# Kernel optimization log

Measured on AMD Instinct MI355X. Metric: run time of the kernel, lower is better.

## Reference

```python
import jax, jax.numpy as jnp
import numpy as np

B, S, HID = 8, 4096, 1024
NH, HD = 16, 64  # heads, head_dim
LN_EPS = 1e-12


def setup_inputs() -> dict:
    key = jax.random.key(0)
    ks = jax.random.split(key, 12)
    sd = 1.0 / np.sqrt(HID)
    return {
        "input_tensor": jax.random.normal(ks[0], (B, S, HID), jnp.float32),
        "attention_mask": jnp.ones((B, S), jnp.int32),
        "ln_gamma": jnp.ones((HID,), jnp.float32),
        "ln_beta": jnp.zeros((HID,), jnp.float32),
        "Wq": jax.random.normal(ks[1], (HID, HID), jnp.float32) * sd,
        "bq": jnp.zeros((HID,), jnp.float32),
        "Wk": jax.random.normal(ks[2], (HID, HID), jnp.float32) * sd,
        "bk": jnp.zeros((HID,), jnp.float32),
        "Wv": jax.random.normal(ks[3], (HID, HID), jnp.float32) * sd,
        "bv": jnp.zeros((HID,), jnp.float32),
        "Wo": jax.random.normal(ks[4], (HID, HID), jnp.float32) * sd,
        "bo": jnp.zeros((HID,), jnp.float32),
    }


def _layernorm(x, g, b):
    mu = jnp.mean(x, axis=-1, keepdims=True)
    var = jnp.mean(jnp.square(x - mu), axis=-1, keepdims=True)
    return (x - mu) * jax.lax.rsqrt(var + LN_EPS) * g + b


def reference(input_tensor, attention_mask, ln_gamma, ln_beta,
              Wq, bq, Wk, bk, Wv, bv, Wo, bo):
    # NOTE: attention_mask is accepted but unused, matching the original module.
    x = input_tensor
    x_norm = _layernorm(x, ln_gamma, ln_beta)
    # projections: query from normalized input, key/value from raw input
    q = (x_norm @ Wq.T + bq).reshape(B, S, NH, HD).transpose(0, 2, 1, 3)  # bhsd
    k = (x @ Wk.T + bk).reshape(B, S, NH, HD).transpose(0, 2, 1, 3)      # bhsd
    v = (x @ Wv.T + bv).reshape(B, S, NH, HD).transpose(0, 2, 1, 3)      # bhsd

    eq = jax.nn.elu(q)
    ek = jax.nn.elu(k)
    # per-token L2 norms over head_dim (matches norm over d in both layouts)
    eq = eq / jnp.linalg.norm(eq, axis=-1, keepdims=True)
    ek = ek / jnp.linalg.norm(ek, axis=-1, keepdims=True)

    # linear attention: Q (K^T V), never materializing [S,S]
    kv = jnp.einsum('bhsd,bhse->bhde', ek, v)          # [B,H,d,d]
    ctx = jnp.einsum('bhsd,bhde->bhse', eq, kv) / np.sqrt(HD)

    ctx = ctx.transpose(0, 2, 1, 3).reshape(B, S, HID)
    out = ctx @ Wo.T + bo
    return out + x  # residual (dropouts are identity in eval mode)
```

## Files before the change

kernel.cpp:

```cpp
#include <hip/hip_runtime.h>

typedef unsigned short u16;
typedef unsigned int   u32;
typedef __attribute__((ext_vector_type(8))) __bf16 bf16x8;
typedef __attribute__((ext_vector_type(4))) float  f32x4;

#define BQ   8
#define SQ   4096
#define NHQ  16
#define HIDD 1024
#define TOKN 32768

__device__ __forceinline__ u16 f2bf(float f){
  u32 u = __builtin_bit_cast(u32, f);
  u += 0x7fffu + ((u >> 16) & 1u);
  return (u16)(u >> 16);
}
__device__ __forceinline__ float bf2f(u16 h){
  return __builtin_bit_cast(float, (u32)h << 16);
}
__device__ __forceinline__ void gl16(const void* g, void* l){
  __builtin_amdgcn_global_load_lds((const __attribute__((address_space(1))) void*)g,
                                   (__attribute__((address_space(3))) void*)l, 16, 0, 0);
}
#define MFMA(a,b,c) __builtin_amdgcn_mfma_f32_16x16x32_bf16((a),(b),(c),0,0,0)

__global__ __launch_bounds__(256) void k_cast4(const float* __restrict__ wq,
    const float* __restrict__ wk, const float* __restrict__ wv, const float* __restrict__ wo,
    u16* __restrict__ oq, u16* __restrict__ okv, u16* __restrict__ oo){
  const int sel = blockIdx.x >> 10;
  const int i = ((blockIdx.x & 1023) << 8) + threadIdx.x;
  const float* in = (sel == 0) ? wq : (sel == 1) ? wk : (sel == 2) ? wv : wo;
  u16* o = (sel == 0) ? oq : (sel == 1) ? okv : (sel == 2) ? (okv + 1024 * 1024) : oo;
  float4 v = ((const float4*)in)[i];
  ushort4 r;
  r.x = f2bf(v.x); r.y = f2bf(v.y); r.z = f2bf(v.z); r.w = f2bf(v.w);
  ((ushort4*)o)[i] = r;
}

__global__ __launch_bounds__(256) void k_ln(const float* __restrict__ x, const float* __restrict__ g,
    const float* __restrict__ be, u16* __restrict__ xbf, u16* __restrict__ xnbf){
  const int row = blockIdx.x, t = threadIdx.x;
  const float4 v = ((const float4*)(x + (size_t)row * HIDD))[t];
  float s  = v.x + v.y + v.z + v.w;
  float ss = v.x*v.x + v.y*v.y + v.z*v.z + v.w*v.w;
  #pragma unroll
  for (int o = 1; o < 64; o <<= 1){ s += __shfl_xor(s, o); ss += __shfl_xor(ss, o); }
  __shared__ float sm[8];
  const int lane = t & 63, wid = t >> 6;
  if (lane == 0){ sm[wid] = s; sm[wid + 4] = ss; }
  __syncthreads();
  s  = sm[0] + sm[1] + sm[2] + sm[3];
  ss = sm[4] + sm[5] + sm[6] + sm[7];
  const float mu   = s * (1.f / 1024.f);
  const float var  = ss * (1.f / 1024.f) - mu * mu;
  const float rstd = rsqrtf(var + 1e-12f);
  const float4 gg = ((const float4*)g)[t];
  const float4 bb = ((const float4*)be)[t];
  ushort4 xo, no;
  xo.x = f2bf(v.x); no.x = f2bf((v.x - mu) * rstd * gg.x + bb.x);
  xo.y = f2bf(v.y); no.y = f2bf((v.y - mu) * rstd * gg.y + bb.y);
  xo.z = f2bf(v.z); no.z = f2bf((v.z - mu) * rstd * gg.z + bb.z);
  xo.w = f2bf(v.w); no.w = f2bf((v.w - mu) * rstd * gg.w + bb.w);
  ((ushort4*)(xbf  + (size_t)row * HIDD))[t] = xo;
  ((ushort4*)(xnbf + (size_t)row * HIDD))[t] = no;
}

struct GP {
  const u16* A; const u16* W; const float* b1; const float* b2;
  int nsplit, lgNB, LDC, nblk; u16* outb;
};

template<int RES>
__global__ __launch_bounds__(512, 2) void k_gemm256(GP p0, GP p1, int seg0,
    const float* __restrict__ resid, float* __restrict__ outf){
  __shared__ union {
    u16 st[2][2][16384];
    float cep[8][1056];
  } sm;

  const GP& p = (blockIdx.x < seg0) ? p0 : p1;
  const int bseg = (blockIdx.x < seg0) ? blockIdx.x : blockIdx.x - seg0;
  const u16* __restrict__ A = p.A;
  const u16* __restrict__ W = p.W;
  const int lgNB = p.lgNB, LDC = p.LDC;

  const int wg = ((bseg & 7) * (p.nblk >> 3)) + (bseg >> 3);
  const int m0 = (wg >> lgNB) << 8;
  const int n0 = (wg & ((1 << lgNB) - 1)) << 8;

  const int t = threadIdx.x, lane = t & 63, wid = t >> 6;
  const int ln15 = lane & 15, hi = lane >> 4;
  const int wr = wid >> 2, wc = wid & 3;
  const int lg = lane & 7, lr = lane >> 3;

  auto stage = [&](int buf, int op, const u16* __restrict__ src, int rowoff, int kt){
    #pragma unroll
    for (int i = 0; i < 4; i++){
      const int cb  = ((i << 3) + wid) << 6;
      const int row = (cb >> 3) + lr;
      const int g   = lg ^ lr;
      gl16(src + (size_t)(rowoff + row) * HIDD + (kt << 6) + (g << 3),
           &sm.st[buf][op][cb << 3]);
    }
  };
  #define RD_A(c,m,ks) (*(const bf16x8*)&sm.st[c][0][(((wr << 7) + ((m) << 4) + ln15) << 6) + \
      (((((ks) << 2) + hi) ^ (lane & 7)) << 3)])
  #define RD_B(c,n,ks) (*(const bf16x8*)&sm.st[c][1][(((wc << 6) + ((n) << 4) + ln15) << 6) + \
      (((((ks) << 2) + hi) ^ (lane & 7)) << 3)])

  f32x4 acc[8][4] = {};

  stage(0, 0, A, m0, 0);
  stage(0, 1, W, n0, 0);
  stage(1, 1, W, n0, 1);
  asm volatile("s_waitcnt vmcnt(4)" ::: "memory");
  __builtin_amdgcn_s_barrier();
  asm volatile("" ::: "memory");

  const int NT = HIDD / 64;
  for (int kt = 0; kt < NT; ++kt){
    const int c = kt & 1;
    bf16x8 af[4][2], bq[4][2];
    #pragma unroll
    for (int m = 0; m < 4; m++){ af[m][0] = RD_A(c, m, 0); af[m][1] = RD_A(c, m, 1); }
    #pragma unroll
    for (int n = 0; n < 4; n++){ bq[n][0] = RD_B(c, n, 0); bq[n][1] = RD_B(c, n, 1); }
    const int ka = kt + 1 < NT ? kt + 1 : NT - 1;
    stage(c ^ 1, 0, A, m0, ka);
    __builtin_amdgcn_s_setprio(1);
    #pragma unroll
    for (int m = 0; m < 4; m++)
      #pragma unroll
      for (int n = 0; n < 4; n++){
        acc[m][n] = MFMA(af[m][0], bq[n][0], acc[m][n]);
        acc[m][n] = MFMA(af[m][1], bq[n][1], acc[m][n]);
      }
    __builtin_amdgcn_s_setprio(0);
    asm volatile("" ::: "memory");
    __builtin_amdgcn_s_barrier();
    asm volatile("" ::: "memory");
    #pragma unroll
    for (int m = 0; m < 4; m++){ af[m][0] = RD_A(c, m + 4, 0); af[m][1] = RD_A(c, m + 4, 1); }
    const int kb = kt + 2 < NT ? kt + 2 : NT - 1;
    stage(c, 1, W, n0, kb);
    __builtin_amdgcn_s_setprio(1);
    #pragma unroll
    for (int m = 0; m < 4; m++)
      #pragma unroll
      for (int n = 0; n < 4; n++){
        acc[m + 4][n] = MFMA(af[m][0], bq[n][0], acc[m + 4][n]);
        acc[m + 4][n] = MFMA(af[m][1], bq[n][1], acc[m + 4][n]);
      }
    __builtin_amdgcn_s_setprio(0);
    asm volatile("s_waitcnt vmcnt(4)" ::: "memory");
    __builtin_amdgcn_s_barrier();
    asm volatile("" ::: "memory");
  }
  #undef RD_A
  #undef RD_B

  asm volatile("s_waitcnt vmcnt(0)" ::: "memory");
  __builtin_amdgcn_s_barrier();
  asm volatile("" ::: "memory");

  const float* bp = (n0 < p.nsplit) ? p.b1 : (p.b2 - p.nsplit);
  float bn[4];
  #pragma unroll
  for (int n = 0; n < 4; n++) bn[n] = bp[n0 + (wc << 6) + (n << 4) + ln15];

  if constexpr (RES){
    #pragma unroll
    for (int m = 0; m < 8; m++)
      #pragma unroll
      for (int n = 0; n < 4; n++)
        #pragma unroll
        for (int r = 0; r < 4; r++){
          int row = m0 + (wr << 7) + (m << 4) + (hi << 2) + r;
          int col = n0 + (wc << 6) + (n << 4) + ln15;
          outf[(size_t)row * LDC + col] = acc[m][n][r] + bn[n]
                                        + resid[(size_t)row * HIDD + col];
        }
  } else {
    float* cw = &sm.cep[wid][0];
    const int rr = lane >> 3, cb8 = (lane & 7) << 3;
    u16* outb = p.outb;
    #pragma unroll
    for (int m = 0; m < 8; m++){
      #pragma unroll
      for (int n = 0; n < 4; n++)
        #pragma unroll
        for (int r = 0; r < 4; r++)
          cw[((hi << 2) + r) * 66 + (n << 4) + ln15] = acc[m][n][r] + bn[n];
      #pragma unroll
      for (int j = 0; j < 2; j++){
        const int row = (j << 3) + rr;
        u32 ro[4];
        #pragma unroll
        for (int pq = 0; pq < 4; pq++){
          float v0 = cw[row * 66 + cb8 + 2 * pq];
          float v1 = cw[row * 66 + cb8 + 2 * pq + 1];
          ro[pq] = (u32)f2bf(v0) | ((u32)f2bf(v1) << 16);
        }
        uint4 o; o.x = ro[0]; o.y = ro[1]; o.z = ro[2]; o.w = ro[3];
        *(uint4*)&outb[(size_t)(m0 + (wr << 7) + (m << 4) + row) * LDC
                       + n0 + (wc << 6) + cb8] = o;
      }
    }
  }
}

__global__ __launch_bounds__(256) void k_elunorm(u16* __restrict__ q){
  size_t idx = (size_t)blockIdx.x * 256 + threadIdx.x;
  uint4 u = ((const uint4*)q)[idx];
  u32 uu[4] = {u.x, u.y, u.z, u.w};
  float e[8]; float ss = 0.f;
  #pragma unroll
  for (int i = 0; i < 4; i++){
    float f0 = bf2f((u16)(uu[i] & 0xffff));
    float f1 = bf2f((u16)(uu[i] >> 16));
    f0 = f0 > 0.f ? f0 : expm1f(f0);
    f1 = f1 > 0.f ? f1 : expm1f(f1);
    e[2*i] = f0; e[2*i+1] = f1;
    ss += f0 * f0 + f1 * f1;
  }
  ss += __shfl_xor(ss, 1); ss += __shfl_xor(ss, 2); ss += __shfl_xor(ss, 4);
  float rn = rsqrtf(ss);
  u32 ro[4];
  #pragma unroll
  for (int i = 0; i < 4; i++)
    ro[i] = (u32)f2bf(e[2*i] * rn) | ((u32)f2bf(e[2*i+1] * rn) << 16);
  uint4 o; o.x = ro[0]; o.y = ro[1]; o.z = ro[2]; o.w = ro[3];
  ((uint4*)q)[idx] = o;
}

__global__ __launch_bounds__(256) void k_transpose2(const u16* __restrict__ kvb,
                                                    u16* __restrict__ ekT, u16* __restrict__ vT){
  __shared__ float tile[64][65];
  __shared__ float pr[64][4];
  __shared__ float rn[64];
  const int sb = blockIdx.x << 6, h2 = blockIdx.y, b = blockIdx.z;
  const int h = h2 & 15;
  const int isK = (h2 >> 4) == 0;
  const u16* in = kvb + ((h2 >> 4) << 10);
  u16* outp = isK ? ekT : vT;
  const int t = threadIdx.x;
  {
    const int tok = t >> 2, q = t & 3;
    const u16* src = in + (size_t)(b * SQ + sb + tok) * 2048 + (h << 6) + (q << 4);
    uint4 u0 = *(const uint4*)src;
    uint4 u1 = *(const uint4*)(src + 8);
    u32 uu[8] = {u0.x, u0.y, u0.z, u0.w, u1.x, u1.y, u1.z, u1.w};
    float ss = 0.f;
    #pragma unroll
    for (int i = 0; i < 8; i++){
      float f0 = bf2f((u16)(uu[i] & 0xffff));
      float f1 = bf2f((u16)(uu[i] >> 16));
      if (isK){
        f0 = f0 > 0.f ? f0 : expm1f(f0);
        f1 = f1 > 0.f ? f1 : expm1f(f1);
        ss += f0 * f0 + f1 * f1;
      }
      tile[tok][(q << 4) + 2*i]     = f0;
      tile[tok][(q << 4) + 2*i + 1] = f1;
    }
    if (isK) pr[tok][q] = ss;
  }
  __syncthreads();
  if (isK){
    if (t < 64) rn[t] = rsqrtf(pr[t][0] + pr[t][1] + pr[t][2] + pr[t][3]);
    __syncthreads();
  }
  const int d = t >> 2, sq2 = (t & 3) << 4;
  u16* dst = outp + ((size_t)(b * NHQ + h) * 64 + d) * SQ + sb + sq2;
  u32 ro[8];
  #pragma unroll
  for (int i = 0; i < 8; i++){
    float v0 = tile[sq2 + 2*i][d];
    float v1 = tile[sq2 + 2*i + 1][d];
    if (isK){ v0 *= rn[sq2 + 2*i]; v1 *= rn[sq2 + 2*i + 1]; }
    ro[i] = (u32)f2bf(v0) | ((u32)f2bf(v1) << 16);
  }
  uint4 o0; o0.x = ro[0]; o0.y = ro[1]; o0.z = ro[2]; o0.w = ro[3];
  uint4 o1; o1.x = ro[4]; o1.y = ro[5]; o1.z = ro[6]; o1.w = ro[7];
  *(uint4*)dst = o0;
  *(uint4*)(dst + 8) = o1;
}

__global__ __launch_bounds__(256) void k_kv(const u16* __restrict__ vT, const u16* __restrict__ ekT,
                                            u16* __restrict__ kvT){
  const int bh = blockIdx.x;
  const u16* Av = vT  + (size_t)bh * 64 * SQ;
  const u16* Bk = ekT + (size_t)bh * 64 * SQ;
  const int lane = threadIdx.x & 63, wid = threadIdx.x >> 6;
  const int ln15 = lane & 15, hi = lane >> 4;
  f32x4 acc[4][4] = {};
  const int kb = wid << 10;
  for (int ks = 0; ks < 32; ++ks){
    const int k0 = kb + (ks << 5) + (hi << 3);
    bf16x8 af[4], bfr[4];
    #pragma unroll
    for (int m = 0; m < 4; m++) af[m]  = *(const bf16x8*)(Av + (size_t)((m << 4) + ln15) * SQ + k0);
    #pragma unroll
    for (int n = 0; n < 4; n++) bfr[n] = *(const bf16x8*)(Bk + (size_t)((n << 4) + ln15) * SQ + k0);
    #pragma unroll
    for (int m = 0; m < 4; m++)
      #pragma unroll
      for (int n = 0; n < 4; n++)
        acc[m][n] = MFMA(af[m], bfr[n], acc[m][n]);
  }
  __shared__ float red[64][64];
  for (int w = 0; w < 4; ++w){
    if (wid == w){
      #pragma unroll
      for (int m = 0; m < 4; m++)
        #pragma unroll
        for (int n = 0; n < 4; n++)
          #pragma unroll
          for (int r = 0; r < 4; r++){
            int row = (m << 4) + (hi << 2) + r;
            int col = (n << 4) + ln15;
            if (w == 0) red[row][col] = acc[m][n][r];
            else        red[row][col] += acc[m][n][r];
          }
    }
    __syncthreads();
  }
  u16* dst = kvT + (size_t)bh * 4096;
  const int tt = threadIdx.x;
  #pragma unroll
  for (int i = 0; i < 16; i++){
    int idx = tt * 16 + i;
    dst[idx] = f2bf(red[idx >> 6][idx & 63] * 0.125f);
  }
}

__global__ __launch_bounds__(256) void k_ctx(const u16* __restrict__ eq, const u16* __restrict__ kvT,
                                             u16* __restrict__ ctx){
  __shared__ u16 Alds[1024 * 8];
  __shared__ u16 Blds[512 * 8];
  const int sb = blockIdx.x << 7;
  const int h = blockIdx.y, b = blockIdx.z;
  const int bh = (b << 4) + h;
  const int t = threadIdx.x, lane = t & 63, wid = t >> 6;
  const int ln15 = lane & 15, hi = lane >> 4;
  {
    uint4 va[4]; uint4 vb[2];
    #pragma unroll
    for (int i = 0; i < 4; i++){
      int c = (wid << 6) + (i << 8) + lane;
      int g = c >> 7, row = c & 127;
      va[i] = *(const uint4*)(eq + (size_t)(b * SQ + sb + row) * HIDD + (h << 6) + g * 8);
    }
    #pragma unroll
    for (int i = 0; i < 2; i++){
      int c = (wid << 6) + (i << 8) + lane;
      int g = c >> 6, row = c & 63;
      vb[i] = *(const uint4*)(kvT + (size_t)bh * 4096 + (row << 6) + g * 8);
    }
    #pragma unroll
    for (int i = 0; i < 4; i++)
      *(uint4*)&Alds[((wid << 6) + (i << 8) + lane) * 8] = va[i];
    #pragma unroll
    for (int i = 0; i < 2; i++)
      *(uint4*)&Blds[((wid << 6) + (i << 8) + lane) * 8] = vb[i];
  }
  __syncthreads();
  f32x4 acc[2][4] = {};
  #pragma unroll
  for (int k2 = 0; k2 < 2; k2++){
    const int g = (k2 << 2) + hi;
    bf16x8 af[2], bfr[4];
    #pragma unroll
    for (int m = 0; m < 2; m++) af[m]  = *(const bf16x8*)&Alds[((g << 7) + (wid << 5) + (m << 4) + ln15) * 8];
    #pragma unroll
    for (int n = 0; n < 4; n++) bfr[n] = *(const bf16x8*)&Blds[((g << 6) + (n << 4) + ln15) * 8];
    #pragma unroll
    for (int m = 0; m < 2; m++)
      #pragma unroll
      for (int n = 0; n < 4; n++)
        acc[m][n] = MFMA(af[m], bfr[n], acc[m][n]);
  }
  #pragma unroll
  for (int m = 0; m < 2; m++)
    #pragma unroll
    for (int n = 0; n < 4; n++)
      #pragma unroll
      for (int r = 0; r < 4; r++){
        int srow = sb + (wid << 5) + (m << 4) + (hi << 2) + r;
        int col  = (n << 4) + ln15;
        ctx[(size_t)(b * SQ + srow) * HIDD + (h << 6) + col] = f2bf(acc[m][n][r]);
      }
}

extern "C" void kernel_launch(void* const* d_in, const int* in_sizes, int n_in,
                              void* d_out, int out_size, void* d_ws, size_t ws_size,
                              hipStream_t stream){
  const float* x   = (const float*)d_in[0];
  const float* lng = (const float*)d_in[2];
  const float* lnb = (const float*)d_in[3];
  const float* Wq  = (const float*)d_in[4];
  const float* bq  = (const float*)d_in[5];
  const float* Wk  = (const float*)d_in[6];
  const float* bk  = (const float*)d_in[7];
  const float* Wv  = (const float*)d_in[8];
  const float* bv  = (const float*)d_in[9];
  const float* Wo  = (const float*)d_in[10];
  const float* bo  = (const float*)d_in[11];
  float* out = (float*)d_out;

  char* w = (char*)d_ws;
  const size_t MB = 1ull << 20;
  u16* wqb  = (u16*)(w + 0   * MB);
  u16* wkvb = (u16*)(w + 2   * MB);
  u16* wob  = (u16*)(w + 6   * MB);
  u16* xbf  = (u16*)(w + 8   * MB);
  u16* xnbf = (u16*)(w + 72  * MB);
  u16* qb   = (u16*)(w + 136 * MB);
  u16* kvb  = (u16*)(w + 200 * MB);
  u16* kvT  = (u16*)(w + 328 * MB);
  u16* ekT = xnbf;
  u16* vT  = xbf;
  u16* ctx = kvb;

  k_cast4<<<4096, 256, 0, stream>>>(Wq, Wk, Wv, Wo, wqb, wkvb, wob);
  k_ln<<<TOKN, 256, 0, stream>>>(x, lng, lnb, xbf, xnbf);

  GP pq  = { xnbf, wqb,  bq, bq, 1 << 30, 2, 1024, 512,  qb  };
  GP pkv = { xbf,  wkvb, bk, bv, 1024,    3, 2048, 1024, kvb };
  k_gemm256<0><<<1536, 512, 0, stream>>>(pq, pkv, 512, nullptr, nullptr);

  k_elunorm<<<16384, 256, 0, stream>>>(qb);
  k_transpose2<<<dim3(64, 32, 8), 256, 0, stream>>>(kvb, ekT, vT);
  k_kv<<<128, 256, 0, stream>>>(vT, ekT, kvT);
  k_ctx<<<dim3(32, 16, 8), 256, 0, stream>>>(qb, kvT, ctx);

  GP po = { ctx, wob, bo, bo, 1 << 30, 2, 1024, 512, nullptr };
  k_gemm256<1><<<512, 512, 0, stream>>>(po, po, 512, x, out);

  (void)in_sizes; (void)n_in; (void)out_size; (void)ws_size;
}
```

Measured before the change: 745.0 us.

## Shrink GEMM tile to 256x128 with K=32 steps for higher occupancy

Changes the bf16 MFMA GEMM from 256x256 tiles with K=64 stages to 256x128 tiles with K=32 stages. LDS drops from 64KB to 48KB, and launch bounds move to 4 blocks per CU. The grids double and the staging/swizzle, pipeline waits and epilogue are rewritten to match. The aim is more concurrent blocks and better latency hiding, at the cost of lower arithmetic intensity per tile and twice as many barriers per K.

```diff
diff --git a/kernel.cpp b/kernel.cpp
--- a/kernel.cpp
+++ b/kernel.cpp
@@ -72,11 +72,11 @@
 };
 
 template<int RES>
-__global__ __launch_bounds__(512, 2) void k_gemm256(GP p0, GP p1, int seg0,
+__global__ __launch_bounds__(512, 4) void k_gemm(GP p0, GP p1, int seg0,
     const float* __restrict__ resid, float* __restrict__ outf){
   __shared__ union {
-    u16 st[2][2][16384];
-    float cep[8][1056];
+    struct { u16 A[2][8192]; u16 B[2][4096]; } st;
+    float cep[8][544];
   } sm;
 
   const GP& p = (blockIdx.x < seg0) ? p0 : p1;
@@ -87,127 +87,104 @@
 
   const int wg = ((bseg & 7) * (p.nblk >> 3)) + (bseg >> 3);
   const int m0 = (wg >> lgNB) << 8;
-  const int n0 = (wg & ((1 << lgNB) - 1)) << 8;
+  const int n0 = (wg & ((1 << lgNB) - 1)) << 7;
 
   const int t = threadIdx.x, lane = t & 63, wid = t >> 6;
   const int ln15 = lane & 15, hi = lane >> 4;
   const int wr = wid >> 2, wc = wid & 3;
-  const int lg = lane & 7, lr = lane >> 3;
-
-  auto stage = [&](int buf, int op, const u16* __restrict__ src, int rowoff, int kt){
-    #pragma unroll
-    for (int i = 0; i < 4; i++){
-      const int cb  = ((i << 3) + wid) << 6;
-      const int row = (cb >> 3) + lr;
-      const int g   = lg ^ lr;
-      gl16(src + (size_t)(rowoff + row) * HIDD + (kt << 6) + (g << 3),
-           &sm.st[buf][op][cb << 3]);
+
+  auto stage = [&](int buf, int kt){
+    #pragma unroll
+    for (int i = 0; i < 2; i++){
+      const int c = (i << 9) + t;
+      const int row = c >> 2, g = c & 3;
+      gl16(A + (size_t)(m0 + row) * HIDD + (kt << 5) + ((g ^ (row & 3)) << 3),
+           &sm.st.A[buf][c << 3]);
+    }
+    {
+      const int c = t;
+      const int row = c >> 2, g = c & 3;
+      gl16(W + (size_t)(n0 + row) * HIDD + (kt << 5) + ((g ^ (row & 3)) << 3),
+           &sm.st.B[buf][c << 3]);
     }
   };
-  #define RD_A(c,m,ks) (*(const bf16x8*)&sm.st[c][0][(((wr << 7) + ((m) << 4) + ln15) << 6) + \
-      (((((ks) << 2) + hi) ^ (lane & 7)) << 3)])
-  #define RD_B(c,n,ks) (*(const bf16x8*)&sm.st[c][1][(((wc << 6) + ((n) << 4) + ln15) << 6) + \
-      (((((ks) << 2) + hi) ^ (lane & 7)) << 3)])
-
-  f32x4 acc[8][4] = {};
-
-  stage(0, 0, A, m0, 0);
-  stage(0, 1, W, n0, 0);
-  stage(1, 1, W, n0, 1);
-  asm volatile("s_waitcnt vmcnt(4)" ::: "memory");
-  __builtin_amdgcn_s_barrier();
-  asm volatile("" ::: "memory");
-
-  const int NT = HIDD / 64;
+  #define RD_A(cb,m) (*(const bf16x8*)&sm.st.A[cb][(((wr << 7) + ((m) << 4) + ln15) << 5) + \
+      ((hi ^ (ln15 & 3)) << 3)])
+  #define RD_B(cb,n) (*(const bf16x8*)&sm.st.B[cb][(((wc << 5) + ((n) << 4) + ln15) << 5) + \
+      ((hi ^ (ln15 & 3)) << 3)])
+
+  f32x4 acc[8][2] = {};
+  stage(0, 0); stage(1, 1);
+
+  const int NT = HIDD / 32;
   for (int kt = 0; kt < NT; ++kt){
-    const int c = kt & 1;
-    bf16x8 af[4][2], bq[4][2];
-    #pragma unroll
-    for (int m = 0; m < 4; m++){ af[m][0] = RD_A(c, m, 0); af[m][1] = RD_A(c, m, 1); }
-    #pragma unroll
-    for (int n = 0; n < 4; n++){ bq[n][0] = RD_B(c, n, 0); bq[n][1] = RD_B(c, n, 1); }
-    const int ka = kt + 1 < NT ? kt + 1 : NT - 1;
-    stage(c ^ 1, 0, A, m0, ka);
+    const int cb = kt & 1;
+    asm volatile("s_waitcnt vmcnt(3)" ::: "memory");
+    __builtin_amdgcn_s_barrier();
+    asm volatile("" ::: "memory");
+    bf16x8 af[8], bq[2];
+    #pragma unroll
+    for (int m = 0; m < 8; m++) af[m] = RD_A(cb, m);
+    #pragma unroll
+    for (int n = 0; n < 2; n++) bq[n] = RD_B(cb, n);
     __builtin_amdgcn_s_setprio(1);
     #pragma unroll
-    for (int m = 0; m < 4; m++)
-      #pragma unroll
-      for (int n = 0; n < 4; n++){
-        acc[m][n] = MFMA(af[m][0], bq[n][0], acc[m][n]);
-        acc[m][n] = MFMA(af[m][1], bq[n][1], acc[m][n]);
-      }
+    for (int m = 0; m < 8; m++)
+      #pragma unroll
+      for (int n = 0; n < 2; n++)
+        acc[m][n] = MFMA(af[m], bq[n], acc[m][n]);
     __builtin_amdgcn_s_setprio(0);
     asm volatile("" ::: "memory");
     __builtin_amdgcn_s_barrier();
     asm volatile("" ::: "memory");
-    #pragma unroll
-    for (int m = 0; m < 4; m++){ af[m][0] = RD_A(c, m + 4, 0); af[m][1] = RD_A(c, m + 4, 1); }
-    const int kb = kt + 2 < NT ? kt + 2 : NT - 1;
-    stage(c, 1, W, n0, kb);
-    __builtin_amdgcn_s_setprio(1);
-    #pragma unroll
-    for (int m = 0; m < 4; m++)
-      #pragma unroll
-      for (int n = 0; n < 4; n++){
-        acc[m + 4][n] = MFMA(af[m][0], bq[n][0], acc[m + 4][n]);
-        acc[m + 4][n] = MFMA(af[m][1], bq[n][1], acc[m + 4][n]);
-      }
-    __builtin_amdgcn_s_setprio(0);
-    asm volatile("s_waitcnt vmcnt(4)" ::: "memory");
-    __builtin_amdgcn_s_barrier();
-    asm volatile("" ::: "memory");
-  }
-  #undef RD_A
-  #undef RD_B
-
+    stage(cb, kt + 2 < NT ? kt + 2 : NT - 1);
+  }
   asm volatile("s_waitcnt vmcnt(0)" ::: "memory");
   __builtin_amdgcn_s_barrier();
   asm volatile("" ::: "memory");
 
   const float* bp = (n0 < p.nsplit) ? p.b1 : (p.b2 - p.nsplit);
-  float bn[4];
-  #pragma unroll
-  for (int n = 0; n < 4; n++) bn[n] = bp[n0 + (wc << 6) + (n << 4) + ln15];
+  float bn[2];
+  #pragma unroll
+  for (int n = 0; n < 2; n++) bn[n] = bp[n0 + (wc << 5) + (n << 4) + ln15];
 
   if constexpr (RES){
     #pragma unroll
     for (int m = 0; m < 8; m++)
       #pragma unroll
-      for (int n = 0; n < 4; n++)
+      for (int n = 0; n < 2; n++)
         #pragma unroll
         for (int r = 0; r < 4; r++){
           int row = m0 + (wr << 7) + (m << 4) + (hi << 2) + r;
-          int col = n0 + (wc << 6) + (n << 4) + ln15;
+          int col = n0 + (wc << 5) + (n << 4) + ln15;
           outf[(size_t)row * LDC + col] = acc[m][n][r] + bn[n]
                                         + resid[(size_t)row * HIDD + col];
         }
   } else {
     float* cw = &sm.cep[wid][0];
-    const int rr = lane >> 3, cb8 = (lane & 7) << 3;
+    const int rr = lane >> 2, cb8 = (lane & 3) << 3;
     u16* outb = p.outb;
     #pragma unroll
     for (int m = 0; m < 8; m++){
       #pragma unroll
-      for (int n = 0; n < 4; n++)
+      for (int n = 0; n < 2; n++)
         #pragma unroll
         for (int r = 0; r < 4; r++)
-          cw[((hi << 2) + r) * 66 + (n << 4) + ln15] = acc[m][n][r] + bn[n];
-      #pragma unroll
-      for (int j = 0; j < 2; j++){
-        const int row = (j << 3) + rr;
-        u32 ro[4];
-        #pragma unroll
-        for (int pq = 0; pq < 4; pq++){
-          float v0 = cw[row * 66 + cb8 + 2 * pq];
-          float v1 = cw[row * 66 + cb8 + 2 * pq + 1];
-          ro[pq] = (u32)f2bf(v0) | ((u32)f2bf(v1) << 16);
-        }
-        uint4 o; o.x = ro[0]; o.y = ro[1]; o.z = ro[2]; o.w = ro[3];
-        *(uint4*)&outb[(size_t)(m0 + (wr << 7) + (m << 4) + row) * LDC
-                       + n0 + (wc << 6) + cb8] = o;
+          cw[((hi << 2) + r) * 34 + (n << 4) + ln15] = acc[m][n][r] + bn[n];
+      u32 ro[4];
+      #pragma unroll
+      for (int pq = 0; pq < 4; pq++){
+        float v0 = cw[rr * 34 + cb8 + 2 * pq];
+        float v1 = cw[rr * 34 + cb8 + 2 * pq + 1];
+        ro[pq] = (u32)f2bf(v0) | ((u32)f2bf(v1) << 16);
       }
-    }
-  }
+      uint4 o; o.x = ro[0]; o.y = ro[1]; o.z = ro[2]; o.w = ro[3];
+      *(uint4*)&outb[(size_t)(m0 + (wr << 7) + (m << 4) + rr) * LDC
+                     + n0 + (wc << 5) + cb8] = o;
+    }
+  }
+  #undef RD_A
+  #undef RD_B
 }
 
 __global__ __launch_bounds__(256) void k_elunorm(u16* __restrict__ q){
@@ -426,17 +403,17 @@
   k_cast4<<<4096, 256, 0, stream>>>(Wq, Wk, Wv, Wo, wqb, wkvb, wob);
   k_ln<<<TOKN, 256, 0, stream>>>(x, lng, lnb, xbf, xnbf);
 
-  GP pq  = { xnbf, wqb,  bq, bq, 1 << 30, 2, 1024, 512,  qb  };
-  GP pkv = { xbf,  wkvb, bk, bv, 1024,    3, 2048, 1024, kvb };
-  k_gemm256<0><<<1536, 512, 0, stream>>>(pq, pkv, 512, nullptr, nullptr);
+  GP pq  = { xnbf, wqb,  bq, bq, 1 << 30, 3, 1024, 1024, qb  };
+  GP pkv = { xbf,  wkvb, bk, bv, 1024,    4, 2048, 2048, kvb };
+  k_gemm<0><<<3072, 512, 0, stream>>>(pq, pkv, 1024, nullptr, nullptr);
 
   k_elunorm<<<16384, 256, 0, stream>>>(qb);
   k_transpose2<<<dim3(64, 32, 8), 256, 0, stream>>>(kvb, ekT, vT);
   k_kv<<<128, 256, 0, stream>>>(vT, ekT, kvT);
   k_ctx<<<dim3(32, 16, 8), 256, 0, stream>>>(qb, kvT, ctx);
 
-  GP po = { ctx, wob, bo, bo, 1 << 30, 2, 1024, 512, nullptr };
-  k_gemm256<1><<<512, 512, 0, stream>>>(po, po, 512, x, out);
+  GP po = { ctx, wob, bo, bo, 1 << 30, 3, 1024, 1024, nullptr };
+  k_gemm<1><<<1024, 512, 0, stream>>>(po, po, 1024, x, out);
 
   (void)in_sizes; (void)n_in; (void)out_size; (void)ws_size;
 }
```

Result: slower. 918.3 us (+23.3%).

## Fuse ELU+L2-norm of Q into ctx kernel and vectorize residual epilogue

Applied to the files above, without the earlier changes.

Drops the standalone k_elunorm pass over the Q projection and applies ELU plus per-token L2 normalization inside k_ctx, on the tile already staged in LDS. This saves one full read and write of the 64 MB bf16 Q buffer and one kernel launch, at the cost of an extra barrier and some ALU work in k_ctx. Separately, the residual output GEMM epilogue is staged through LDS so residual loads and fp32 output stores become 16-byte vectors instead of scattered scalar accesses.

```diff
diff --git a/kernel.cpp b/kernel.cpp
--- a/kernel.cpp
+++ b/kernel.cpp
@@ -169,21 +169,39 @@
   #pragma unroll
   for (int n = 0; n < 4; n++) bn[n] = bp[n0 + (wc << 6) + (n << 4) + ln15];
 
+  float* cw = &sm.cep[wid][0];
+  const int rr = lane >> 3, cb8 = (lane & 7) << 3;
+
   if constexpr (RES){
     #pragma unroll
-    for (int m = 0; m < 8; m++)
+    for (int m = 0; m < 8; m++){
       #pragma unroll
       for (int n = 0; n < 4; n++)
         #pragma unroll
-        for (int r = 0; r < 4; r++){
-          int row = m0 + (wr << 7) + (m << 4) + (hi << 2) + r;
-          int col = n0 + (wc << 6) + (n << 4) + ln15;
-          outf[(size_t)row * LDC + col] = acc[m][n][r] + bn[n]
-                                        + resid[(size_t)row * HIDD + col];
-        }
+        for (int r = 0; r < 4; r++)
+          cw[((hi << 2) + r) * 66 + (n << 4) + ln15] = acc[m][n][r] + bn[n];
+      #pragma unroll
+      for (int j = 0; j < 2; j++){
+        const int row = (j << 3) + rr;
+        const size_t gr = (size_t)(m0 + (wr << 7) + (m << 4) + row);
+        const size_t gidx = gr * LDC + n0 + (wc << 6) + cb8;
+        const size_t ridx = gr * HIDD + n0 + (wc << 6) + cb8;
+        const float4 ra = *(const float4*)&resid[ridx];
+        const float4 rb = *(const float4*)&resid[ridx + 4];
+        float4 o0, o1;
+        o0.x = cw[row * 66 + cb8 + 0] + ra.x;
+        o0.y = cw[row * 66 + cb8 + 1] + ra.y;
+        o0.z = cw[row * 66 + cb8 + 2] + ra.z;
+        o0.w = cw[row * 66 + cb8 + 3] + ra.w;
+        o1.x = cw[row * 66 + cb8 + 4] + rb.x;
+        o1.y = cw[row * 66 + cb8 + 5] + rb.y;
+        o1.z = cw[row * 66 + cb8 + 6] + rb.z;
+        o1.w = cw[row * 66 + cb8 + 7] + rb.w;
+        *(float4*)&outf[gidx]     = o0;
+        *(float4*)&outf[gidx + 4] = o1;
+      }
+    }
   } else {
-    float* cw = &sm.cep[wid][0];
-    const int rr = lane >> 3, cb8 = (lane & 7) << 3;
     u16* outb = p.outb;
     #pragma unroll
     for (int m = 0; m < 8; m++){
@@ -208,30 +226,6 @@
       }
     }
   }
-}
-
-__global__ __launch_bounds__(256) void k_elunorm(u16* __restrict__ q){
-  size_t idx = (size_t)blockIdx.x * 256 + threadIdx.x;
-  uint4 u = ((const uint4*)q)[idx];
-  u32 uu[4] = {u.x, u.y, u.z, u.w};
-  float e[8]; float ss = 0.f;
-  #pragma unroll
-  for (int i = 0; i < 4; i++){
-    float f0 = bf2f((u16)(uu[i] & 0xffff));
-    float f1 = bf2f((u16)(uu[i] >> 16));
-    f0 = f0 > 0.f ? f0 : expm1f(f0);
-    f1 = f1 > 0.f ? f1 : expm1f(f1);
-    e[2*i] = f0; e[2*i+1] = f1;
-    ss += f0 * f0 + f1 * f1;
-  }
-  ss += __shfl_xor(ss, 1); ss += __shfl_xor(ss, 2); ss += __shfl_xor(ss, 4);
-  float rn = rsqrtf(ss);
-  u32 ro[4];
-  #pragma unroll
-  for (int i = 0; i < 4; i++)
-    ro[i] = (u32)f2bf(e[2*i] * rn) | ((u32)f2bf(e[2*i+1] * rn) << 16);
-  uint4 o; o.x = ro[0]; o.y = ro[1]; o.z = ro[2]; o.w = ro[3];
-  ((uint4*)q)[idx] = o;
 }
 
 __global__ __launch_bounds__(256) void k_transpose2(const u16* __restrict__ kvb,
@@ -335,10 +329,11 @@
   }
 }
 
-__global__ __launch_bounds__(256) void k_ctx(const u16* __restrict__ eq, const u16* __restrict__ kvT,
+__global__ __launch_bounds__(256) void k_ctx(const u16* __restrict__ q, const u16* __restrict__ kvT,
                                              u16* __restrict__ ctx){
   __shared__ u16 Alds[1024 * 8];
   __shared__ u16 Blds[512 * 8];
+  __shared__ float prn[128][2];
   const int sb = blockIdx.x << 7;
   const int h = blockIdx.y, b = blockIdx.z;
   const int bh = (b << 4) + h;
@@ -350,7 +345,7 @@
     for (int i = 0; i < 4; i++){
       int c = (wid << 6) + (i << 8) + lane;
       int g = c >> 7, row = c & 127;
-      va[i] = *(const uint4*)(eq + (size_t)(b * SQ + sb + row) * HIDD + (h << 6) + g * 8);
+      va[i] = *(const uint4*)(q + (size_t)(b * SQ + sb + row) * HIDD + (h << 6) + g * 8);
     }
     #pragma unroll
     for (int i = 0; i < 2; i++){
@@ -364,6 +359,39 @@
     #pragma unroll
     for (int i = 0; i < 2; i++)
       *(uint4*)&Blds[((wid << 6) + (i << 8) + lane) * 8] = vb[i];
+  }
+  __syncthreads();
+  {
+    const int row = t & 127, half = t >> 7;
+    float vals[4][8]; float ss = 0.f;
+    #pragma unroll
+    for (int g4 = 0; g4 < 4; g4++){
+      const int g = (half << 2) + g4;
+      uint4 u = *(const uint4*)&Alds[((g << 7) + row) * 8];
+      u32 uu[4] = {u.x, u.y, u.z, u.w};
+      #pragma unroll
+      for (int i = 0; i < 4; i++){
+        float f0 = bf2f((u16)(uu[i] & 0xffff));
+        float f1 = bf2f((u16)(uu[i] >> 16));
+        f0 = f0 > 0.f ? f0 : expm1f(f0);
+        f1 = f1 > 0.f ? f1 : expm1f(f1);
+        vals[g4][2*i] = f0; vals[g4][2*i+1] = f1;
+        ss += f0 * f0 + f1 * f1;
+      }
+    }
+    prn[row][half] = ss;
+    __syncthreads();
+    const float rn = rsqrtf(prn[row][0] + prn[row][1]);
+    #pragma unroll
+    for (int g4 = 0; g4 < 4; g4++){
+      const int g = (half << 2) + g4;
+      u32 ro[4];
+      #pragma unroll
+      for (int i = 0; i < 4; i++)
+        ro[i] = (u32)f2bf(vals[g4][2*i] * rn) | ((u32)f2bf(vals[g4][2*i+1] * rn) << 16);
+      uint4 o; o.x = ro[0]; o.y = ro[1]; o.z = ro[2]; o.w = ro[3];
+      *(uint4*)&Alds[((g << 7) + row) * 8] = o;
+    }
   }
   __syncthreads();
   f32x4 acc[2][4] = {};
@@ -430,7 +458,6 @@
   GP pkv = { xbf,  wkvb, bk, bv, 1024,    3, 2048, 1024, kvb };
   k_gemm256<0><<<1536, 512, 0, stream>>>(pq, pkv, 512, nullptr, nullptr);
 
-  k_elunorm<<<16384, 256, 0, stream>>>(qb);
   k_transpose2<<<dim3(64, 32, 8), 256, 0, stream>>>(kvb, ekT, vT);
   k_kv<<<128, 256, 0, stream>>>(vT, ekT, kvT);
   k_ctx<<<dim3(32, 16, 8), 256, 0, stream>>>(qb, kvT, ctx);
```

Result: faster. 693.0 us (-7.0%).
